# Performance work log

Measured on AMD Instinct MI355X. Metric: run time of the kernel, lower is better.

The kernel has to match this reference:

```python
import jax, jax.numpy as jnp
import numpy as np

BS = 16; N_PER = 1024; N = BS * N_PER; K = 9; E = N * K
H = 128; NODE_D = 64; EDGE_D = 16; RBF_DIM = 20; R_CUT = 1.0; L = 4; SF = 0.1


def setup_inputs():
    ks = jax.random.split(jax.random.key(0), 24)
    X = jax.random.normal(ks[0], (N, 3), dtype=jnp.float32) * 0.5
    node_attr = jax.random.normal(ks[1], (N, NODE_D), dtype=jnp.float32)
    edge_attr = jax.random.normal(ks[2], (E, EDGE_D), dtype=jnp.float32)
    idx = jnp.arange(N, dtype=jnp.int32)
    bid = idx // N_PER
    Seg = ((idx % N_PER) >= (N_PER // 2)).astype(jnp.int32)
    row = jnp.repeat(idx, K)
    col = (row // N_PER) * N_PER + jax.random.randint(ks[3], (E,), 0, N_PER, dtype=jnp.int32)
    edges = jnp.stack([row, col])

    def g(k, shape, fan):
        return jax.random.normal(k, shape, dtype=jnp.float32) * (1.0 / float(np.sqrt(fan)))

    MI = 2 * H + RBF_DIM + EDGE_D  # message MLP input dim
    return {
        'X': X, 'node_attr': node_attr, 'edge_attr': edge_attr,
        'W_in1': g(ks[4], (NODE_D, H), NODE_D), 'b_in1': jnp.zeros((H,), jnp.float32),
        'W_in2': g(ks[5], (H, H), H), 'b_in2': jnp.zeros((H,), jnp.float32),
        'We1': g(ks[6], (L, MI, H), MI), 'be1': jnp.zeros((L, H), jnp.float32),
        'We2': g(ks[7], (L, H, H), H), 'be2': jnp.zeros((L, H), jnp.float32),
        'Wv': g(ks[8], (L, H, H), H), 'Wvv': g(ks[9], (L, H, H), H),
        'Wh1': g(ks[10], (L, 2 * H, H), 2 * H), 'bh1': jnp.zeros((L, H), jnp.float32),
        'Wh2': g(ks[11], (L, H, H), H), 'bh2': jnp.zeros((L, H), jnp.float32),
        'Wi1': g(ks[12], (L, H, H), H), 'bi1': jnp.zeros((L, H), jnp.float32),
        'Wi2': g(ks[13], (L, H, H), H), 'bi2': jnp.zeros((L, H), jnp.float32),
        'Wgv1': g(ks[14], (H, H), H), 'Wgv2': g(ks[15], (H, H), H),
        'Wg1': g(ks[16], (2 * H, H), 2 * H), 'bg1': jnp.zeros((H,), jnp.float32),
        'Wg2': g(ks[17], (H, 2 * H), H), 'bg2': jnp.zeros((2 * H,), jnp.float32),
        'Wf': g(ks[18], (H, 9), H),
        'edges': edges, 'Seg': Seg, 'bid': bid,
    }


def _fwd(X, node_attr, edge_attr, W_in1, b_in1, W_in2, b_in2, We1, be1, We2, be2, Wv, Wvv, Wh1, bh1, Wh2, bh2, Wi1, bi1, Wi2, bi2, Wgv1, Wgv2, Wg1, bg1, Wg2, bg2, Wf, edges, Seg, bid):
    silu = jax.nn.silu
    row, col = edges[0], edges[1]
    nseg = 2 * BS
    seg_id = bid * 2 + Seg  # (complex, receptor/ligand) segment id
    # coord2radial + Bessel RBF with cosine cutoff
    diff = X[row] - X[col]
    norm = jnp.sqrt(jnp.sum(diff * diff, axis=-1)) + 1e-8
    unit = diff / norm[:, None]
    freqs = jnp.arange(1, RBF_DIM + 1, dtype=X.dtype) * (jnp.pi / R_CUT)
    rbf = jnp.sin(norm[:, None] * freqs[None, :]) / norm[:, None]
    cut = 0.5 * (jnp.cos(jnp.pi * jnp.clip(norm, 0.0, R_CUT) / R_CUT) + 1.0)
    rbf = rbf * cut[:, None]
    # in_conv
    h = silu(node_attr @ W_in1 + b_in1) @ W_in2 + b_in2
    v = jnp.zeros((N, H, 3), dtype=h.dtype)
    counts = jax.ops.segment_sum(jnp.ones((N,), dtype=h.dtype), seg_id, num_segments=nseg)
    opp = bid * 2 + (1 - Seg)  # opposite-molecule segment per node
    for i in range(L):
        # PINN message passing (PaiNN-style equivariant layer)
        m_in = jnp.concatenate([h[row], h[col], rbf, edge_attr], axis=-1)
        m = silu(m_in @ We1[i] + be1[i]) @ We2[i] + be2[i]  # [E, H]
        agg = jax.ops.segment_sum(m, row, num_segments=N)
        h_intra = h + silu(jnp.concatenate([h, agg], axis=-1) @ Wh1[i] + bh1[i]) @ Wh2[i] + bh2[i]
        v_msg = (m @ Wv[i])[:, :, None] * unit[:, None, :] + (m @ Wvv[i])[:, :, None] * v[col]
        v = v + jax.ops.segment_sum(v_msg, row, num_segments=N)
        # cross receptor<->ligand softmax attention: (H_a @ H_b.T).mean(1) == H_a @ mean(H_b)
        mean_h = jax.ops.segment_sum(h_intra, seg_id, num_segments=nseg) / counts[:, None]
        score = jnp.sum(h_intra * mean_h[opp], axis=-1)
        smax = jax.ops.segment_max(score, seg_id, num_segments=nseg)
        ex = jnp.exp(score - smax[seg_id])
        w = ex / jax.ops.segment_sum(ex, seg_id, num_segments=nseg)[seg_id]
        gated = h_intra * w[:, None]
        h = h_intra + silu(gated @ Wi1[i] + bi1[i]) @ Wi2[i] + bi2[i]
    # gated equivariant block
    v1 = jnp.einsum('nhc,hk->nkc', v, Wgv1)
    v2 = jnp.einsum('nhc,hk->nkc', v, Wgv2)
    v2n = jnp.sqrt(jnp.sum(v2 * v2, axis=-1) + 1e-8)
    mix = silu(jnp.concatenate([h, v2n], axis=-1) @ Wg1 + bg1) @ Wg2 + bg2
    h, bgate = mix[:, :H], mix[:, H:]
    v = v1 * bgate[:, :, None]
    # final_conv + per-(complex, molecule) pooled prediction vectors [2*BS, 9, 3]
    pv = jnp.einsum('nhc,ho->noc', v * h[:, :, None], Wf)
    pred = jax.ops.segment_sum(pv.reshape(N, 27), seg_id, num_segments=nseg).reshape(nseg, 9, 3)
    # kron/outer-product quadratic surface params: A [., 3, 3], b [., 3]
    A = (pred[:, 0, :, None] * pred[:, 1, None, :] + pred[:, 3, :, None] * pred[:, 2, None, :]
         + pred[:, 4, :, None] * pred[:, 5, None, :] + pred[:, 7, :, None] * pred[:, 6, None, :]) / (SF * SF)
    bvec = pred[:, 8] / SF
    return jnp.concatenate([A, bvec[:, :, None]], axis=2)  # [2*BS, 3, 4]


def reference(X, node_attr, edge_attr, W_in1, b_in1, W_in2, b_in2, We1, be1, We2, be2, Wv, Wvv, Wh1, bh1, Wh2, bh2, Wi1, bi1, Wi2, bi2, Wgv1, Wgv2, Wg1, bg1, Wg2, bg2, Wf, edges, Seg, bid):
    return _fwd(X, node_attr, edge_attr, W_in1, b_in1, W_in2, b_in2, We1, be1, We2, be2, Wv, Wvv, Wh1, bh1, Wh2, bh2, Wi1, bi1, Wi2, bi2, Wgv1, Wgv2, Wg1, bg1, Wg2, bg2, Wf, edges, Seg, bid)
```

## Files before the change

kernel.cpp:

```cpp
#include <hip/hip_runtime.h>
#include <math.h>

#define NN 16384
#define NE 147456
#define NSEGS 32
#define HD 128
#define RBF_D 20
#define EDGE_DD 16
#define NODE_DD 64
#define NLAYER 4
#define PI_F 3.14159265358979323846f


typedef __attribute__((ext_vector_type(8))) short v8s;
typedef __attribute__((ext_vector_type(4))) float v4f;
typedef __attribute__((ext_vector_type(8))) unsigned short v8u;

__device__ __forceinline__ unsigned short f2bf(float f) {
  union { float f; unsigned int u; } x; x.f = f;
  unsigned int u = x.u;
  return (unsigned short)((u + 0x7FFFu + ((u >> 16) & 1u)) >> 16);
}
__device__ __forceinline__ float bf2f(unsigned short b) {
  union { unsigned int u; float f; } x; x.u = ((unsigned int)b) << 16; return x.f;
}
__device__ __forceinline__ void split8(float4 a, float4 b, v8u& hi, v8u& lo) {
  float v[8] = {a.x, a.y, a.z, a.w, b.x, b.y, b.z, b.w};
#pragma unroll
  for (int i = 0; i < 8; i++) {
    unsigned short h = f2bf(v[i]);
    hi[i] = h;
    lo[i] = f2bf(v[i] - bf2f(h));
  }
}
__device__ __forceinline__ float silu_f(float v) { return v / (1.f + expf(-v)); }

struct WDesc { const float* src; const float* src2; unsigned short* hi; unsigned short* lo;
               int K; int N; int Kp; int ld; };
struct WDescs { WDesc d[48]; };
__global__ void wconv_k(WDescs ds) {
  WDesc d = ds.d[blockIdx.y];
  int idx = blockIdx.x * 256 + threadIdx.x;
  if (idx >= d.N * d.Kp) return;
  int n = idx / d.Kp, k = idx - n * d.Kp;
  const float* s = d.src; int nn = n;
  if (d.src2 && n >= 128) { s = d.src2; nn = n - 128; }
  float v = (k < d.K) ? s[(size_t)k * d.ld + nn] : 0.f;
  unsigned short h = f2bf(v);
  d.hi[idx] = h;
  d.lo[idx] = f2bf(v - bf2f(h));
}

__global__ void wcomb_k(const float* __restrict__ We2, const float* __restrict__ Wv,
                        const float* __restrict__ Wvv, float* __restrict__ Wc) {
  int l = blockIdx.z, which = blockIdx.y, xb = blockIdx.x;
  const float* A = We2 + (size_t)l * 128 * 128;
  const float* B = (which ? Wvv : Wv) + (size_t)l * 128 * 128;
  float* D = Wc + ((size_t)(which * NLAYER + l)) * 128 * 128;
  int n = threadIdx.x & 127, r2 = threadIdx.x >> 7;
#pragma unroll
  for (int i = 0; i < 8; i++) {
    int k1 = xb * 16 + r2 * 8 + i;
    float s = 0.f;
    for (int j = 0; j < 128; j++) s += A[k1 * 128 + j] * B[j * 128 + n];
    D[(size_t)k1 * 128 + n] = s;
  }
}
__global__ void bcomb_k(const float* __restrict__ be2, const float* __restrict__ Wv,
                        const float* __restrict__ Wvv, const float* __restrict__ be1,
                        float* __restrict__ bcv, float* __restrict__ bcvv,
                        float* __restrict__ b9, float* __restrict__ bx) {
  int l = blockIdx.x, n = threadIdx.x;
  const float* b = be2 + l * 128;
  float sv = 0.f, svv = 0.f;
  for (int j = 0; j < 128; j++) {
    sv  += b[j] * Wv[(size_t)l * 16384 + j * 128 + n];
    svv += b[j] * Wvv[(size_t)l * 16384 + j * 128 + n];
  }
  bcv[l * 128 + n] = sv; bcvv[l * 128 + n] = svv; b9[l * 128 + n] = 9.f * b[n];
  bx[l * 256 + n] = be1[l * 128 + n]; bx[l * 256 + 128 + n] = 0.f;
}

constexpr int LDS_S = 40;

template<int BM, int AMODE, int OUTM, int RESM>
__global__ __launch_bounds__(256, 2)
void mgemm_k(const float* A0f, const unsigned short* Ah0, const unsigned short* Al0,
             const unsigned short* __restrict__ Wth, const unsigned short* __restrict__ Wtl,
             int Kp, const float* __restrict__ bias, const float* __restrict__ resf,
             float* Cf, int ldc, unsigned short* Ch, unsigned short* Cl, int lda)
{
  constexpr int MT = BM / 32;
  __shared__ unsigned short Ah[BM * LDS_S], Al[BM * LDS_S];
  __shared__ unsigned short Bh[128 * LDS_S], Bl[128 * LDS_S];
  const int tid = threadIdx.x;
  const int m0 = blockIdx.x * BM;
  const int coff = blockIdx.y * 128;
  const int w = tid >> 6, lane = tid & 63;
  const int lm = lane & 15, kq = lane >> 4;
  const int wm = (w >> 1) * (BM / 2);
  const int wn = (w & 1) * 64;

  v4f acc[MT][4];
#pragma unroll
  for (int i = 0; i < MT; i++)
#pragma unroll
    for (int j = 0; j < 4; j++) acc[i][j] = (v4f){0.f, 0.f, 0.f, 0.f};

  const int KT = Kp >> 5;
  for (int kt = 0; kt < KT; kt++) {
#pragma unroll
    for (int i = 0; i < BM / 64; i++) {
      int m = i * 64 + (tid >> 2);
      int k8 = (tid & 3) * 8;
      int gk = kt * 32 + k8, gm = m0 + m;
      v8u hi, lo;
      if constexpr (AMODE == 1) {
        hi = *(const v8u*)&Ah0[(size_t)gm * 128 + gk];
        lo = *(const v8u*)&Al0[(size_t)gm * 128 + gk];
      } else {
        float4 a = *(const float4*)&A0f[(size_t)gm * lda + gk];
        float4 b = *(const float4*)&A0f[(size_t)gm * lda + gk + 4];
        split8(a, b, hi, lo);
      }
      *(v8u*)&Ah[m * LDS_S + k8] = hi;
      *(v8u*)&Al[m * LDS_S + k8] = lo;
    }
#pragma unroll
    for (int i = 0; i < 2; i++) {
      int f = i * 256 + tid;
      int n = f >> 2, k8 = (f & 3) * 8;
      size_t g = (size_t)(coff + n) * Kp + kt * 32 + k8;
      *(v8u*)&Bh[n * LDS_S + k8] = *(const v8u*)&Wth[g];
      *(v8u*)&Bl[n * LDS_S + k8] = *(const v8u*)&Wtl[g];
    }
    __syncthreads();
    v8s afh[MT], afl[MT];
#pragma unroll
    for (int mi = 0; mi < MT; mi++) {
      int r = wm + mi * 16 + lm;
      afh[mi] = *(v8s*)&Ah[r * LDS_S + kq * 8];
      afl[mi] = *(v8s*)&Al[r * LDS_S + kq * 8];
    }
#pragma unroll
    for (int ni = 0; ni < 4; ni++) {
      int r = wn + ni * 16 + lm;
      v8s bh = *(v8s*)&Bh[r * LDS_S + kq * 8];
      v8s bl = *(v8s*)&Bl[r * LDS_S + kq * 8];
#pragma unroll
      for (int mi = 0; mi < MT; mi++) {
        acc[mi][ni] = __builtin_amdgcn_mfma_f32_16x16x32_bf16(afh[mi], bh, acc[mi][ni], 0, 0, 0);
        acc[mi][ni] = __builtin_amdgcn_mfma_f32_16x16x32_bf16(afl[mi], bh, acc[mi][ni], 0, 0, 0);
        acc[mi][ni] = __builtin_amdgcn_mfma_f32_16x16x32_bf16(afh[mi], bl, acc[mi][ni], 0, 0, 0);
      }
    }
    __syncthreads();
  }
#pragma unroll
  for (int mi = 0; mi < MT; mi++) {
#pragma unroll
    for (int r = 0; r < 4; r++) {
      int mrow = m0 + wm + mi * 16 + kq * 4 + r;
#pragma unroll
      for (int ni = 0; ni < 4; ni++) {
        int ncol = coff + wn + ni * 16 + lm;
        float v = acc[mi][ni][r];
        if constexpr (RESM == 3) v += bias[ncol] * resf[mrow];
        else { if (bias) v += bias[ncol]; }
        if constexpr (OUTM == 0) Cf[(size_t)mrow * ldc + ncol] = v;
        else if constexpr (OUTM == 1) {
          unsigned short h = f2bf(v);
          Ch[(size_t)mrow * 128 + ncol] = h;
          Cl[(size_t)mrow * 128 + ncol] = f2bf(v - bf2f(h));
        } else {
          Ch[(size_t)mrow * 128 + ncol] = f2bf(v);
        }
      }
    }
  }
}

__device__ __forceinline__ float4 loadRE(const float* __restrict__ rbf,
                                         const float* __restrict__ ea, int m, int k4) {
  if (k4 < RBF_D) return *(const float4*)&rbf[(size_t)m * RBF_D + k4];
  if (k4 < RBF_D + EDGE_DD) return *(const float4*)&ea[(size_t)m * EDGE_DD + k4 - RBF_D];
  return make_float4(0.f, 0.f, 0.f, 0.f);
}

__global__ __launch_bounds__(256, 4)
void mrev_k(const float* __restrict__ rbf, const float* __restrict__ ea,
            const float* __restrict__ hrc, const float* __restrict__ unitv,
            const int* __restrict__ gcol,
            const unsigned short* __restrict__ W1h, const unsigned short* __restrict__ W1l,
            const unsigned short* __restrict__ W2h, const unsigned short* __restrict__ W2l,
            const float* __restrict__ bcvv,
            float* __restrict__ agg, float* __restrict__ U,
            unsigned short* __restrict__ mvvh)
{
  __shared__ unsigned short Th[64 * 136], Tl[64 * 136];
  __shared__ float su[192];
  unsigned short* Ah = Th;
  unsigned short* Al = Th + 64 * LDS_S;
  const int tid = threadIdx.x;
  const int m0 = blockIdx.x * 64;
  const int w = tid >> 6, lane = tid & 63;
  const int lm = lane & 15, kq = lane >> 4;
  const int wm = (w >> 1) * 32, wn = (w & 1) * 64;

  if (tid < 192) su[tid] = unitv[(size_t)m0 * 3 + tid];

  v4f acc[2][4];
#pragma unroll
  for (int i = 0; i < 2; i++)
#pragma unroll
    for (int j = 0; j < 4; j++) acc[i][j] = (v4f){0.f, 0.f, 0.f, 0.f};

  for (int kt = 0; kt < 2; kt++) {
    {
      int m = tid >> 2, k8 = (tid & 3) * 8;
      int gk = kt * 32 + k8, gm = m0 + m;
      v8u hi, lo;
      split8(loadRE(rbf, ea, gm, gk), loadRE(rbf, ea, gm, gk + 4), hi, lo);
      *(v8u*)&Ah[m * LDS_S + k8] = hi;
      *(v8u*)&Al[m * LDS_S + k8] = lo;
    }
    __syncthreads();
    v8s afh[2], afl[2];
#pragma unroll
    for (int mi = 0; mi < 2; mi++) {
      int r = wm + mi * 16 + lm;
      afh[mi] = *(v8s*)&Ah[r * LDS_S + kq * 8];
      afl[mi] = *(v8s*)&Al[r * LDS_S + kq * 8];
    }
#pragma unroll
    for (int ni = 0; ni < 4; ni++) {
      int n = wn + ni * 16 + lm;
      v8s bh = *(const v8s*)&W1h[(size_t)n * 64 + kt * 32 + kq * 8];
      v8s bl = *(const v8s*)&W1l[(size_t)n * 64 + kt * 32 + kq * 8];
#pragma unroll
      for (int mi = 0; mi < 2; mi++) {
        acc[mi][ni] = __builtin_amdgcn_mfma_f32_16x16x32_bf16(afh[mi], bh, acc[mi][ni], 0, 0, 0);
        acc[mi][ni] = __builtin_amdgcn_mfma_f32_16x16x32_bf16(afl[mi], bh, acc[mi][ni], 0, 0, 0);
        acc[mi][ni] = __builtin_amdgcn_mfma_f32_16x16x32_bf16(afh[mi], bl, acc[mi][ni], 0, 0, 0);
      }
    }
    __syncthreads();
  }
#pragma unroll
  for (int mi = 0; mi < 2; mi++) {
#pragma unroll
    for (int r = 0; r < 4; r++) {
      int row = wm + mi * 16 + kq * 4 + r;
      int e = m0 + row;
      const float* pr = hrc + (size_t)(e / 9) * 256;
      const float* pc = hrc + (size_t)gcol[e] * 256 + 128;
#pragma unroll
      for (int ni = 0; ni < 4; ni++) {
        int nc = wn + ni * 16 + lm;
        float v = silu_f(acc[mi][ni][r] + pr[nc] + pc[nc]);
        unsigned short h = f2bf(v);
        Th[row * 136 + nc] = h;
        Tl[row * 136 + nc] = f2bf(v - bf2f(h));
      }
    }
  }
  __syncthreads();
  {
    const size_t P = (size_t)NN * 128;
    int nfirst = m0 / 9;
#pragma unroll
    for (int it = 0; it < 4; it++) {
      int idx = it * 256 + tid;
      int ln = idx >> 7, c = idx & 127;
      int n = nfirst + ln;
      int r0 = n * 9 - m0, r1 = r0 + 9;
      if (r0 < 0) r0 = 0;
      if (r1 > 64) r1 = 64;
      float s = 0.f, u0 = 0.f, u1 = 0.f, u2 = 0.f;
      for (int r = r0; r < r1; r++) {
        float m = bf2f(Th[r * 136 + c]) + bf2f(Tl[r * 136 + c]);
        s += m;
        u0 += su[r * 3 + 0] * m;
        u1 += su[r * 3 + 1] * m;
        u2 += su[r * 3 + 2] * m;
      }
      if (r0 < r1) {
        size_t b = (size_t)n * 128 + c;
        atomicAdd(&agg[b], s);
        atomicAdd(&U[b], u0);
        atomicAdd(&U[P + b], u1);
        atomicAdd(&U[2 * P + b], u2);
      }
    }
  }
  v4f acc2[2][4];
#pragma unroll
  for (int i = 0; i < 2; i++)
#pragma unroll
    for (int j = 0; j < 4; j++) acc2[i][j] = (v4f){0.f, 0.f, 0.f, 0.f};
  for (int kt = 0; kt < 4; kt++) {
    v8s afh[2], afl[2];
#pragma unroll
    for (int mi = 0; mi < 2; mi++) {
      int r = wm + mi * 16 + lm;
      afh[mi] = *(v8s*)&Th[r * 136 + kt * 32 + kq * 8];
      afl[mi] = *(v8s*)&Tl[r * 136 + kt * 32 + kq * 8];
    }
#pragma unroll
    for (int ni = 0; ni < 4; ni++) {
      int n = wn + ni * 16 + lm;
      v8s bh = *(const v8s*)&W2h[(size_t)n * 128 + kt * 32 + kq * 8];
      v8s bl = *(const v8s*)&W2l[(size_t)n * 128 + kt * 32 + kq * 8];
#pragma unroll
      for (int mi = 0; mi < 2; mi++) {
        acc2[mi][ni] = __builtin_amdgcn_mfma_f32_16x16x32_bf16(afh[mi], bh, acc2[mi][ni], 0, 0, 0);
        acc2[mi][ni] = __builtin_amdgcn_mfma_f32_16x16x32_bf16(afl[mi], bh, acc2[mi][ni], 0, 0, 0);
        acc2[mi][ni] = __builtin_amdgcn_mfma_f32_16x16x32_bf16(afh[mi], bl, acc2[mi][ni], 0, 0, 0);
      }
    }
  }
#pragma unroll
  for (int mi = 0; mi < 2; mi++) {
#pragma unroll
    for (int r = 0; r < 4; r++) {
      int e = m0 + wm + mi * 16 + kq * 4 + r;
#pragma unroll
      for (int ni = 0; ni < 4; ni++) {
        int nc = wn + ni * 16 + lm;
        mvvh[(size_t)e * 128 + nc] = f2bf(acc2[mi][ni][r] + bcvv[nc]);
      }
    }
  }
}

template<int AMODE, int OUTM, int RESM>
__global__ __launch_bounds__(256, 2)
void mlp2_k(const float* A0f, const float* A1f,
            const unsigned short* Ah0, const unsigned short* Al0,
            const unsigned short* __restrict__ W1h, const unsigned short* __restrict__ W1l,
            int k1p, const float* __restrict__ b1,
            const unsigned short* __restrict__ W2h, const unsigned short* __restrict__ W2l,
            const float* __restrict__ b2,
            const float* resf, const unsigned short* resh, const unsigned short* resl,
            float* Cf, int ldc, unsigned short* Ch, unsigned short* Cl, int lda)
{
  __shared__ unsigned short Ah[64 * LDS_S], Al[64 * LDS_S];
  __shared__ unsigned short Bh[128 * LDS_S], Bl[128 * LDS_S];
  __shared__ unsigned short Th[64 * 136], Tl[64 * 136];
  const int tid = threadIdx.x;
  const int m0 = blockIdx.x * 64;
  const int w = tid >> 6, lane = tid & 63;
  const int lm = lane & 15, kq = lane >> 4;
  const int wm = (w >> 1) * 32, wn = (w & 1) * 64;

  v4f acc[2][4];
#pragma unroll
  for (int i = 0; i < 2; i++)
#pragma unroll
    for (int j = 0; j < 4; j++) acc[i][j] = (v4f){0.f, 0.f, 0.f, 0.f};

  for (int kt = 0; kt < (k1p >> 5); kt++) {
    {
      int m = tid >> 2, k8 = (tid & 3) * 8;
      int gk = kt * 32 + k8, gm = m0 + m;
      v8u hi, lo;
      if constexpr (AMODE == 3) {
        if (gk < 128) {
          hi = *(const v8u*)&Ah0[(size_t)gm * 128 + gk];
          lo = *(const v8u*)&Al0[(size_t)gm * 128 + gk];
        } else {
          float4 a = *(const float4*)&A1f[(size_t)gm * 128 + gk - 128];
          float4 b = *(const float4*)&A1f[(size_t)gm * 128 + gk - 124];
          split8(a, b, hi, lo);
        }
      } else {
        float4 a = *(const float4*)&A0f[(size_t)gm * lda + gk];
        float4 b = *(const float4*)&A0f[(size_t)gm * lda + gk + 4];
        if constexpr (AMODE == 4) {
          float s = A1f[gm];
          a.x *= s; a.y *= s; a.z *= s; a.w *= s;
          b.x *= s; b.y *= s; b.z *= s; b.w *= s;
        }
        split8(a, b, hi, lo);
      }
      *(v8u*)&Ah[m * LDS_S + k8] = hi;
      *(v8u*)&Al[m * LDS_S + k8] = lo;
    }
#pragma unroll
    for (int i = 0; i < 2; i++) {
      int f = i * 256 + tid;
      int n = f >> 2, k8 = (f & 3) * 8;
      size_t g = (size_t)n * k1p + kt * 32 + k8;
      *(v8u*)&Bh[n * LDS_S + k8] = *(const v8u*)&W1h[g];
      *(v8u*)&Bl[n * LDS_S + k8] = *(const v8u*)&W1l[g];
    }
    __syncthreads();
    v8s afh[2], afl[2];
#pragma unroll
    for (int mi = 0; mi < 2; mi++) {
      int r = wm + mi * 16 + lm;
      afh[mi] = *(v8s*)&Ah[r * LDS_S + kq * 8];
      afl[mi] = *(v8s*)&Al[r * LDS_S + kq * 8];
    }
#pragma unroll
    for (int ni = 0; ni < 4; ni++) {
      int r = wn + ni * 16 + lm;
      v8s bh = *(v8s*)&Bh[r * LDS_S + kq * 8];
      v8s bl = *(v8s*)&Bl[r * LDS_S + kq * 8];
#pragma unroll
      for (int mi = 0; mi < 2; mi++) {
        acc[mi][ni] = __builtin_amdgcn_mfma_f32_16x16x32_bf16(afh[mi], bh, acc[mi][ni], 0, 0, 0);
        acc[mi][ni] = __builtin_amdgcn_mfma_f32_16x16x32_bf16(afl[mi], bh, acc[mi][ni], 0, 0, 0);
        acc[mi][ni] = __builtin_amdgcn_mfma_f32_16x16x32_bf16(afh[mi], bl, acc[mi][ni], 0, 0, 0);
      }
    }
    __syncthreads();
  }
#pragma unroll
  for (int mi = 0; mi < 2; mi++) {
#pragma unroll
    for (int r = 0; r < 4; r++) {
      int row = wm + mi * 16 + kq * 4 + r;
#pragma unroll
      for (int ni = 0; ni < 4; ni++) {
        int col = wn + ni * 16 + lm;
        float v = silu_f(acc[mi][ni][r] + b1[col]);
        unsigned short h = f2bf(v);
        Th[row * 136 + col] = h;
        Tl[row * 136 + col] = f2bf(v - bf2f(h));
      }
    }
  }
  __syncthreads();
  const int coff2 = blockIdx.y * 128;
  v4f acc2[2][4];
#pragma unroll
  for (int i = 0; i < 2; i++)
#pragma unroll
    for (int j = 0; j < 4; j++) acc2[i][j] = (v4f){0.f, 0.f, 0.f, 0.f};
  for (int kt = 0; kt < 4; kt++) {
#pragma unroll
    for (int i = 0; i < 2; i++) {
      int f = i * 256 + tid;
      int n = f >> 2, k8 = (f & 3) * 8;
      size_t g = (size_t)(coff2 + n) * 128 + kt * 32 + k8;
      *(v8u*)&Bh[n * LDS_S + k8] = *(const v8u*)&W2h[g];
      *(v8u*)&Bl[n * LDS_S + k8] = *(const v8u*)&W2l[g];
    }
    __syncthreads();
    v8s afh[2], afl[2];
#pragma unroll
    for (int mi = 0; mi < 2; mi++) {
      int r = wm + mi * 16 + lm;
      afh[mi] = *(v8s*)&Th[r * 136 + kt * 32 + kq * 8];
      afl[mi] = *(v8s*)&Tl[r * 136 + kt * 32 + kq * 8];
    }
#pragma unroll
    for (int ni = 0; ni < 4; ni++) {
      int r = wn + ni * 16 + lm;
      v8s bh = *(v8s*)&Bh[r * LDS_S + kq * 8];
      v8s bl = *(v8s*)&Bl[r * LDS_S + kq * 8];
#pragma unroll
      for (int mi = 0; mi < 2; mi++) {
        acc2[mi][ni] = __builtin_amdgcn_mfma_f32_16x16x32_bf16(afh[mi], bh, acc2[mi][ni], 0, 0, 0);
        acc2[mi][ni] = __builtin_amdgcn_mfma_f32_16x16x32_bf16(afl[mi], bh, acc2[mi][ni], 0, 0, 0);
        acc2[mi][ni] = __builtin_amdgcn_mfma_f32_16x16x32_bf16(afh[mi], bl, acc2[mi][ni], 0, 0, 0);
      }
    }
    __syncthreads();
  }
#pragma unroll
  for (int mi = 0; mi < 2; mi++) {
#pragma unroll
    for (int r = 0; r < 4; r++) {
      int mrow = m0 + wm + mi * 16 + kq * 4 + r;
#pragma unroll
      for (int ni = 0; ni < 4; ni++) {
        int ncol = coff2 + wn + ni * 16 + lm;
        float v = acc2[mi][ni][r];
        if (b2) v += b2[ncol];
        if constexpr (RESM == 1) v += resf[(size_t)mrow * 128 + ncol];
        if constexpr (RESM == 2) v += bf2f(resh[(size_t)mrow * 128 + ncol]) + bf2f(resl[(size_t)mrow * 128 + ncol]);
        if constexpr (OUTM == 0) Cf[(size_t)mrow * ldc + ncol] = v;
        else {
          unsigned short h = f2bf(v);
          Ch[(size_t)mrow * 128 + ncol] = h;
          Cl[(size_t)mrow * 128 + ncol] = f2bf(v - bf2f(h));
        }
      }
    }
  }
}

__global__ void edge_geom_k(const float* __restrict__ X, const int* __restrict__ row,
                            const int* __restrict__ col,
                            float* __restrict__ unitv, float* __restrict__ rbf) {
  int e = blockIdx.x * 256 + threadIdx.x;
  if (e >= NE) return;
  int r = row[e], c = col[e];
  float dx = X[r * 3 + 0] - X[c * 3 + 0];
  float dy = X[r * 3 + 1] - X[c * 3 + 1];
  float dz = X[r * 3 + 2] - X[c * 3 + 2];
  float norm = sqrtf(dx * dx + dy * dy + dz * dz) + 1e-8f;
  float inv = 1.f / norm;
  unitv[e * 3 + 0] = dx * inv;
  unitv[e * 3 + 1] = dy * inv;
  unitv[e * 3 + 2] = dz * inv;
  float cl = fminf(norm, 1.0f);
  float cut = 0.5f * (cosf(PI_F * cl) + 1.0f);
  float s = cut * inv;
#pragma unroll
  for (int j = 0; j < RBF_D; j++) rbf[(size_t)e * RBF_D + j] = sinf(norm * (float)(j + 1) * PI_F) * s;
}

__global__ void sup_k(const float* __restrict__ unitv, float* __restrict__ sup) {
  int n = blockIdx.x * 256 + threadIdx.x;
  if (n >= NN) return;
  float q0 = 0.f, q1 = 0.f, q2 = 0.f;
#pragma unroll
  for (int k = 0; k < 9; k++) {
    const float* u = &unitv[(size_t)(n * 9 + k) * 3];
    q0 += u[0]; q1 += u[1]; q2 += u[2];
  }
  sup[n] = q0; sup[NN + n] = q1; sup[2 * NN + n] = q2;
}

__global__ void vupd_k(const float* __restrict__ vold, const float* __restrict__ t1,
                       const unsigned short* __restrict__ mvvh,
                       const int* __restrict__ col, float* __restrict__ vnew) {
  const size_t P = (size_t)NN * 128;
  int t = blockIdx.x * 256 + threadIdx.x;
  int n = t >> 7, hh = t & 127;
  size_t b = (size_t)n * 128 + hh;
  float a0 = vold[b] + t1[b];
  float a1 = vold[P + b] + t1[P + b];
  float a2 = vold[2 * P + b] + t1[2 * P + b];
#pragma unroll
  for (int k = 0; k < 9; k++) {
    int e = n * 9 + k;
    int ce = col[e];
    float mvv = bf2f(mvvh[(size_t)e * 128 + hh]);
    size_t cb = (size_t)ce * 128 + hh;
    a0 += mvv * vold[cb];
    a1 += mvv * vold[P + cb];
    a2 += mvv * vold[2 * P + cb];
  }
  vnew[b] = a0; vnew[P + b] = a1; vnew[2 * P + b] = a2;
}

__global__ void meanp_k(const float* __restrict__ hintra, float* __restrict__ meanp) {
  int q = blockIdx.x, s = blockIdx.y, c = threadIdx.x;
  const float* p = hintra + ((size_t)s * 512 + q * 64) * 128 + c;
// ... 132 lines not shown
  const int* rowp = edges;
  const int* colp = edges + NE;
  float* out = (float*)d_out;

  char* ws = (char*)d_ws;
  size_t o = 0;
  auto ab = [&](size_t bytes) { char* p = ws + o; o += (bytes + 255) & ~(size_t)255; return p; };
  float* unitv  = (float*)ab((size_t)NE * 3 * 4);
  float* rbf    = (float*)ab((size_t)NE * RBF_D * 4);
  float* va     = (float*)ab((size_t)NN * 384 * 4);
  float* vb     = (float*)ab((size_t)NN * 384 * 4);
  unsigned short* mvvh = (unsigned short*)ab((size_t)NE * 128 * 2);
  float* hrc    = (float*)ab((size_t)NN * 256 * 4);
  float* U      = (float*)ab((size_t)3 * NN * 128 * 4);
  float* agg    = (float*)ab((size_t)NN * 128 * 4);
  float* sup    = (float*)ab((size_t)3 * NN * 4);
  float* hintra = (float*)ab((size_t)NN * 128 * 4);
  unsigned short* hbh = (unsigned short*)ab((size_t)NN * 128 * 2);
  unsigned short* hbl = (unsigned short*)ab((size_t)NN * 128 * 2);
  float* meanp  = (float*)ab(NSEGS * 8 * 128 * 4);
  float* scoreb = (float*)ab(NN * 4);
  float* wgt    = (float*)ab(NN * 4);
  float* pred   = (float*)ab(NSEGS * 27 * 4);
  float* Wc     = (float*)ab((size_t)2 * NLAYER * 128 * 128 * 4);
  float* bcv    = (float*)ab(NLAYER * 128 * 4);
  float* bcvv   = (float*)ab(NLAYER * 128 * 4);
  float* b9     = (float*)ab(NLAYER * 128 * 4);
  float* bx     = (float*)ab(NLAYER * 256 * 4);
  unsigned short* wt = (unsigned short*)ab(4 * 1024 * 1024);
  float* v12  = (float*)mvvh;
  float* mixb = (float*)U;

  size_t wo = 0;
  auto walloc = [&](size_t n) { unsigned short* p = wt + wo; wo += n; return p; };
  WDescs wd{};
  int wcnt = 0;
  auto addw = [&](const float* src, const float* src2, int K, int N, int Kp, int ld) {
    size_t sz = (size_t)N * Kp;
    unsigned short* hi = walloc(sz);
    unsigned short* lo = walloc(sz);
    wd.d[wcnt] = WDesc{src, src2, hi, lo, K, N, Kp, ld};
    return wcnt++;
  };
  int iWin1 = addw(W_in1, nullptr, 64, 128, 64, 128);
  int iWin2 = addw(W_in2, nullptr, 128, 128, 128, 128);
  int iWe1rc[NLAYER], iWe1re[NLAYER], iWe2[NLAYER], iWcv[NLAYER], iWcvv[NLAYER],
      iWh1[NLAYER], iWh2[NLAYER], iWi1[NLAYER], iWi2[NLAYER];
  for (int i = 0; i < NLAYER; i++) {
    const float* Wl = We1 + (size_t)i * 292 * 128;
    iWe1rc[i] = addw(Wl, Wl + 128 * 128, 128, 256, 128, 128);
    iWe1re[i] = addw(Wl + 256 * 128, nullptr, 36, 128, 64, 128);
    iWe2[i]   = addw(We2 + (size_t)i * 16384, nullptr, 128, 128, 128, 128);
    iWcv[i]   = addw(Wc + (size_t)i * 16384, nullptr, 128, 128, 128, 128);
    iWcvv[i]  = addw(Wc + (size_t)(NLAYER + i) * 16384, nullptr, 128, 128, 128, 128);
    iWh1[i]   = addw(Wh1 + (size_t)i * 256 * 128, nullptr, 256, 128, 256, 128);
    iWh2[i]   = addw(Wh2 + (size_t)i * 16384, nullptr, 128, 128, 128, 128);
    iWi1[i]   = addw(Wi1 + (size_t)i * 16384, nullptr, 128, 128, 128, 128);
    iWi2[i]   = addw(Wi2 + (size_t)i * 16384, nullptr, 128, 128, 128, 128);
  }
  int iWg1   = addw(Wg1, nullptr, 256, 128, 256, 128);
  int iWg2   = addw(Wg2, nullptr, 128, 256, 128, 256);
  int iWgv12 = addw(Wgv1, Wgv2, 128, 256, 128, 128);

  hipMemsetAsync(va, 0, (size_t)NN * 384 * sizeof(float), stream);
  hipMemsetAsync(pred, 0, NSEGS * 27 * sizeof(float), stream);

  wcomb_k<<<dim3(8, 2, NLAYER), 256, 0, stream>>>(We2, Wv, Wvv, Wc);
  bcomb_k<<<NLAYER, 128, 0, stream>>>(be2, Wv, Wvv, be1, bcv, bcvv, b9, bx);
  wconv_k<<<dim3(128, wcnt), 256, 0, stream>>>(wd);
  edge_geom_k<<<NE / 256, 256, 0, stream>>>(X, rowp, colp, unitv, rbf);
  sup_k<<<NN / 256, 256, 0, stream>>>(unitv, sup);

  auto WH = [&](int idx) { return wd.d[idx].hi; };
  auto WL = [&](int idx) { return wd.d[idx].lo; };

  mlp2_k<0, 1, 0><<<dim3(NN / 64, 1), 256, 0, stream>>>(
      node_attr, nullptr, nullptr, nullptr,
      WH(iWin1), WL(iWin1), 64, b_in1, WH(iWin2), WL(iWin2), b_in2,
      nullptr, nullptr, nullptr, nullptr, 128, hbh, hbl, NODE_DD);

  float* vcur = va;
  float* vnxt = vb;
  for (int i = 0; i < NLAYER; i++) {
    hipMemsetAsync(U, 0, (size_t)4 * NN * 128 * sizeof(float), stream);
    mgemm_k<64, 1, 0, 0><<<dim3(NN / 64, 2), 256, 0, stream>>>(
        nullptr, hbh, hbl, WH(iWe1rc[i]), WL(iWe1rc[i]), 128,
        bx + i * 256, nullptr, hrc, 256, nullptr, nullptr, 0);
    mrev_k<<<NE / 64, 256, 0, stream>>>(rbf, edge_attr, hrc, unitv, colp,
        WH(iWe1re[i]), WL(iWe1re[i]), WH(iWcvv[i]), WL(iWcvv[i]),
        bcvv + i * 128, agg, U, mvvh);
    mgemm_k<64, 0, 0, 0><<<dim3(NN / 64, 1), 256, 0, stream>>>(
        agg, nullptr, nullptr, WH(iWe2[i]), WL(iWe2[i]), 128,
        b9 + i * 128, nullptr, agg, 128, nullptr, nullptr, 128);
    mlp2_k<3, 0, 2><<<dim3(NN / 64, 1), 256, 0, stream>>>(
        nullptr, agg, hbh, hbl,
        WH(iWh1[i]), WL(iWh1[i]), 256, bh1 + i * 128, WH(iWh2[i]), WL(iWh2[i]), bh2 + i * 128,
        nullptr, hbh, hbl, hintra, 128, nullptr, nullptr, 0);
    meanp_k<<<dim3(8, NSEGS), 128, 0, stream>>>(hintra, meanp);
    score2_k<<<NN / 4, 256, 0, stream>>>(hintra, meanp, scoreb);
    softmax_k<<<NSEGS, 512, 0, stream>>>(scoreb, wgt);
    mgemm_k<64, 0, 0, 3><<<dim3(3 * NN / 64, 1), 256, 0, stream>>>(
        U, nullptr, nullptr, WH(iWcv[i]), WL(iWcv[i]), 128,
        bcv + i * 128, sup, U, 128, nullptr, nullptr, 128);
    vupd_k<<<NN * 128 / 256, 256, 0, stream>>>(vcur, U, mvvh, colp, vnxt);
    { float* t = vcur; vcur = vnxt; vnxt = t; }
    mlp2_k<4, 1, 1><<<dim3(NN / 64, 1), 256, 0, stream>>>(
        hintra, wgt, nullptr, nullptr,
        WH(iWi1[i]), WL(iWi1[i]), 128, bi1 + i * 128, WH(iWi2[i]), WL(iWi2[i]), bi2 + i * 128,
        hintra, nullptr, nullptr, nullptr, 128, hbh, hbl, 128);
  }

  mgemm_k<64, 0, 0, 0><<<dim3(3 * NN / 64, 2), 256, 0, stream>>>(
      vcur, nullptr, nullptr, WH(iWgv12), WL(iWgv12), 128,
      nullptr, nullptr, v12, 256, nullptr, nullptr, 128);
  v2n_k<<<NN * 128 / 256, 256, 0, stream>>>(v12, agg);
  mlp2_k<3, 0, 0><<<dim3(NN / 64, 2), 256, 0, stream>>>(
      nullptr, agg, hbh, hbl,
      WH(iWg1), WL(iWg1), 256, bg1, WH(iWg2), WL(iWg2), bg2,
      nullptr, nullptr, nullptr, mixb, 256, nullptr, nullptr, 0);
  pv_k<<<NN / 8, 256, 0, stream>>>(v12, mixb, Wf, pred);
  out_k<<<1, 64, 0, stream>>>(pred, out);
}
```

Before: 1.142 ms.

## Load GEMM fragments directly from global memory, dropping LDS staging and barriers

```diff
diff --git a/kernel.cpp b/kernel.cpp
--- a/kernel.cpp
+++ b/kernel.cpp
@@ -81,83 +81,57 @@
   bx[l * 256 + n] = be1[l * 128 + n]; bx[l * 256 + 128 + n] = 0.f;
 }
 
-constexpr int LDS_S = 40;
-
-template<int BM, int AMODE, int OUTM, int RESM>
-__global__ __launch_bounds__(256, 2)
+template<int AMODE, int OUTM, int RESM>
+__global__ __launch_bounds__(256, 4)
 void mgemm_k(const float* A0f, const unsigned short* Ah0, const unsigned short* Al0,
              const unsigned short* __restrict__ Wth, const unsigned short* __restrict__ Wtl,
              int Kp, const float* __restrict__ bias, const float* __restrict__ resf,
              float* Cf, int ldc, unsigned short* Ch, unsigned short* Cl, int lda)
 {
-  constexpr int MT = BM / 32;
-  __shared__ unsigned short Ah[BM * LDS_S], Al[BM * LDS_S];
-  __shared__ unsigned short Bh[128 * LDS_S], Bl[128 * LDS_S];
-  const int tid = threadIdx.x;
-  const int m0 = blockIdx.x * BM;
+  const int m0 = blockIdx.x * 64;
   const int coff = blockIdx.y * 128;
-  const int w = tid >> 6, lane = tid & 63;
+  const int w = threadIdx.x >> 6, lane = threadIdx.x & 63;
   const int lm = lane & 15, kq = lane >> 4;
-  const int wm = (w >> 1) * (BM / 2);
-  const int wn = (w & 1) * 64;
-
-  v4f acc[MT][4];
-#pragma unroll
-  for (int i = 0; i < MT; i++)
+  const int wm = (w >> 1) * 32, wn = (w & 1) * 64;
+
+  v4f acc[2][4];
+#pragma unroll
+  for (int i = 0; i < 2; i++)
 #pragma unroll
     for (int j = 0; j < 4; j++) acc[i][j] = (v4f){0.f, 0.f, 0.f, 0.f};
 
-  const int KT = Kp >> 5;
-  for (int kt = 0; kt < KT; kt++) {
-#pragma unroll
-    for (int i = 0; i < BM / 64; i++) {
-      int m = i * 64 + (tid >> 2);
-      int k8 = (tid & 3) * 8;
-      int gk = kt * 32 + k8, gm = m0 + m;
-      v8u hi, lo;
+  for (int kt = 0; kt < (Kp >> 5); kt++) {
+    v8s afh[2], afl[2];
+#pragma unroll
+    for (int mi = 0; mi < 2; mi++) {
+      int row = m0 + wm + mi * 16 + lm;
+      int gk = kt * 32 + kq * 8;
       if constexpr (AMODE == 1) {
-        hi = *(const v8u*)&Ah0[(size_t)gm * 128 + gk];
-        lo = *(const v8u*)&Al0[(size_t)gm * 128 + gk];
+        afh[mi] = *(const v8s*)&Ah0[(size_t)row * 128 + gk];
+        afl[mi] = *(const v8s*)&Al0[(size_t)row * 128 + gk];
       } else {
-        float4 a = *(const float4*)&A0f[(size_t)gm * lda + gk];
-        float4 b = *(const float4*)&A0f[(size_t)gm * lda + gk + 4];
+        float4 a = *(const float4*)&A0f[(size_t)row * lda + gk];
+        float4 b = *(const float4*)&A0f[(size_t)row * lda + gk + 4];
+        v8u hi, lo;
         split8(a, b, hi, lo);
-      }
-      *(v8u*)&Ah[m * LDS_S + k8] = hi;
-      *(v8u*)&Al[m * LDS_S + k8] = lo;
-    }
-#pragma unroll
-    for (int i = 0; i < 2; i++) {
-      int f = i * 256 + tid;
-      int n = f >> 2, k8 = (f & 3) * 8;
-      size_t g = (size_t)(coff + n) * Kp + kt * 32 + k8;
-      *(v8u*)&Bh[n * LDS_S + k8] = *(const v8u*)&Wth[g];
-      *(v8u*)&Bl[n * LDS_S + k8] = *(const v8u*)&Wtl[g];
-    }
-    __syncthreads();
-    v8s afh[MT], afl[MT];
-#pragma unroll
-    for (int mi = 0; mi < MT; mi++) {
-      int r = wm + mi * 16 + lm;
-      afh[mi] = *(v8s*)&Ah[r * LDS_S + kq * 8];
-      afl[mi] = *(v8s*)&Al[r * LDS_S + kq * 8];
+        afh[mi] = (v8s)hi; afl[mi] = (v8s)lo;
+      }
     }
 #pragma unroll
     for (int ni = 0; ni < 4; ni++) {
-      int r = wn + ni * 16 + lm;
-      v8s bh = *(v8s*)&Bh[r * LDS_S + kq * 8];
-      v8s bl = *(v8s*)&Bl[r * LDS_S + kq * 8];
-#pragma unroll
-      for (int mi = 0; mi < MT; mi++) {
+      int n = coff + wn + ni * 16 + lm;
+      v8s bh = *(const v8s*)&Wth[(size_t)n * Kp + kt * 32 + kq * 8];
+      v8s bl = *(const v8s*)&Wtl[(size_t)n * Kp + kt * 32 + kq * 8];
+#pragma unroll
+      for (int mi = 0; mi < 2; mi++) {
         acc[mi][ni] = __builtin_amdgcn_mfma_f32_16x16x32_bf16(afh[mi], bh, acc[mi][ni], 0, 0, 0);
         acc[mi][ni] = __builtin_amdgcn_mfma_f32_16x16x32_bf16(afl[mi], bh, acc[mi][ni], 0, 0, 0);
         acc[mi][ni] = __builtin_amdgcn_mfma_f32_16x16x32_bf16(afh[mi], bl, acc[mi][ni], 0, 0, 0);
       }
     }
-    __syncthreads();
-  }
-#pragma unroll
-  for (int mi = 0; mi < MT; mi++) {
+  }
+#pragma unroll
+  for (int mi = 0; mi < 2; mi++) {
 #pragma unroll
     for (int r = 0; r < 4; r++) {
       int mrow = m0 + wm + mi * 16 + kq * 4 + r;
@@ -168,12 +142,10 @@
         if constexpr (RESM == 3) v += bias[ncol] * resf[mrow];
         else { if (bias) v += bias[ncol]; }
         if constexpr (OUTM == 0) Cf[(size_t)mrow * ldc + ncol] = v;
-        else if constexpr (OUTM == 1) {
+        else {
           unsigned short h = f2bf(v);
           Ch[(size_t)mrow * 128 + ncol] = h;
           Cl[(size_t)mrow * 128 + ncol] = f2bf(v - bf2f(h));
-        } else {
-          Ch[(size_t)mrow * 128 + ncol] = f2bf(v);
         }
       }
     }
@@ -199,8 +171,6 @@
 {
   __shared__ unsigned short Th[64 * 136], Tl[64 * 136];
   __shared__ float su[192];
-  unsigned short* Ah = Th;
-  unsigned short* Al = Th + 64 * LDS_S;
   const int tid = threadIdx.x;
   const int m0 = blockIdx.x * 64;
   const int w = tid >> 6, lane = tid & 63;
@@ -215,22 +185,16 @@
 #pragma unroll
     for (int j = 0; j < 4; j++) acc[i][j] = (v4f){0.f, 0.f, 0.f, 0.f};
 
+#pragma unroll
   for (int kt = 0; kt < 2; kt++) {
-    {
-      int m = tid >> 2, k8 = (tid & 3) * 8;
-      int gk = kt * 32 + k8, gm = m0 + m;
+    v8s afh[2], afl[2];
+#pragma unroll
+    for (int mi = 0; mi < 2; mi++) {
+      int row = m0 + wm + mi * 16 + lm;
+      int gk = kt * 32 + kq * 8;
       v8u hi, lo;
-      split8(loadRE(rbf, ea, gm, gk), loadRE(rbf, ea, gm, gk + 4), hi, lo);
-      *(v8u*)&Ah[m * LDS_S + k8] = hi;
-      *(v8u*)&Al[m * LDS_S + k8] = lo;
-    }
-    __syncthreads();
-    v8s afh[2], afl[2];
-#pragma unroll
-    for (int mi = 0; mi < 2; mi++) {
-      int r = wm + mi * 16 + lm;
-      afh[mi] = *(v8s*)&Ah[r * LDS_S + kq * 8];
-      afl[mi] = *(v8s*)&Al[r * LDS_S + kq * 8];
+      split8(loadRE(rbf, ea, row, gk), loadRE(rbf, ea, row, gk + 4), hi, lo);
+      afh[mi] = (v8s)hi; afl[mi] = (v8s)lo;
     }
 #pragma unroll
     for (int ni = 0; ni < 4; ni++) {
@@ -244,7 +208,6 @@
         acc[mi][ni] = __builtin_amdgcn_mfma_f32_16x16x32_bf16(afh[mi], bl, acc[mi][ni], 0, 0, 0);
       }
     }
-    __syncthreads();
   }
 #pragma unroll
   for (int mi = 0; mi < 2; mi++) {
@@ -274,6 +237,7 @@
       int ln = idx >> 7, c = idx & 127;
       int n = nfirst + ln;
       int r0 = n * 9 - m0, r1 = r0 + 9;
+      bool interior = (r0 >= 0) && (r1 <= 64);
       if (r0 < 0) r0 = 0;
       if (r1 > 64) r1 = 64;
       float s = 0.f, u0 = 0.f, u1 = 0.f, u2 = 0.f;
@@ -286,10 +250,14 @@
       }
       if (r0 < r1) {
         size_t b = (size_t)n * 128 + c;
-        atomicAdd(&agg[b], s);
-        atomicAdd(&U[b], u0);
-        atomicAdd(&U[P + b], u1);
-        atomicAdd(&U[2 * P + b], u2);
+        if (interior) {
+          agg[b] = s; U[b] = u0; U[P + b] = u1; U[2 * P + b] = u2;
+        } else {
+          atomicAdd(&agg[b], s);
+          atomicAdd(&U[b], u0);
+          atomicAdd(&U[P + b], u1);
+          atomicAdd(&U[2 * P + b], u2);
+        }
       }
     }
   }
@@ -334,7 +302,7 @@
 }
 
 template<int AMODE, int OUTM, int RESM>
-__global__ __launch_bounds__(256, 2)
+__global__ __launch_bounds__(256, 4)
 void mlp2_k(const float* A0f, const float* A1f,
             const unsigned short* Ah0, const unsigned short* Al0,
             const unsigned short* __restrict__ W1h, const unsigned short* __restrict__ W1l,
@@ -344,8 +312,6 @@
             const float* resf, const unsigned short* resh, const unsigned short* resl,
             float* Cf, int ldc, unsigned short* Ch, unsigned short* Cl, int lda)
 {
-  __shared__ unsigned short Ah[64 * LDS_S], Al[64 * LDS_S];
-  __shared__ unsigned short Bh[128 * LDS_S], Bl[128 * LDS_S];
   __shared__ unsigned short Th[64 * 136], Tl[64 * 136];
   const int tid = threadIdx.x;
   const int m0 = blockIdx.x * 64;
@@ -360,53 +326,38 @@
     for (int j = 0; j < 4; j++) acc[i][j] = (v4f){0.f, 0.f, 0.f, 0.f};
 
   for (int kt = 0; kt < (k1p >> 5); kt++) {
-    {
-      int m = tid >> 2, k8 = (tid & 3) * 8;
-      int gk = kt * 32 + k8, gm = m0 + m;
-      v8u hi, lo;
+    v8s afh[2], afl[2];
+#pragma unroll
+    for (int mi = 0; mi < 2; mi++) {
+      int row = m0 + wm + mi * 16 + lm;
+      int gk = kt * 32 + kq * 8;
       if constexpr (AMODE == 3) {
         if (gk < 128) {
-          hi = *(const v8u*)&Ah0[(size_t)gm * 128 + gk];
-          lo = *(const v8u*)&Al0[(size_t)gm * 128 + gk];
+          afh[mi] = *(const v8s*)&Ah0[(size_t)row * 128 + gk];
+          afl[mi] = *(const v8s*)&Al0[(size_t)row * 128 + gk];
         } else {
-          float4 a = *(const float4*)&A1f[(size_t)gm * 128 + gk - 128];
-          float4 b = *(const float4*)&A1f[(size_t)gm * 128 + gk - 124];
-          split8(a, b, hi, lo);
+          float4 a = *(const float4*)&A1f[(size_t)row * 128 + gk - 128];
+          float4 b = *(const float4*)&A1f[(size_t)row * 128 + gk - 124];
+          v8u hi, lo; split8(a, b, hi, lo);
+          afh[mi] = (v8s)hi; afl[mi] = (v8s)lo;
         }
       } else {
-        float4 a = *(const float4*)&A0f[(size_t)gm * lda + gk];
-        float4 b = *(const float4*)&A0f[(size_t)gm * lda + gk + 4];
+        float4 a = *(const float4*)&A0f[(size_t)row * lda + gk];
+        float4 b = *(const float4*)&A0f[(size_t)row * lda + gk + 4];
         if constexpr (AMODE == 4) {
-          float s = A1f[gm];
+          float s = A1f[row];
           a.x *= s; a.y *= s; a.z *= s; a.w *= s;
           b.x *= s; b.y *= s; b.z *= s; b.w *= s;
         }
-        split8(a, b, hi, lo);
-      }
-      *(v8u*)&Ah[m * LDS_S + k8] = hi;
-      *(v8u*)&Al[m * LDS_S + k8] = lo;
-    }
-#pragma unroll
-    for (int i = 0; i < 2; i++) {
-      int f = i * 256 + tid;
-      int n = f >> 2, k8 = (f & 3) * 8;
-      size_t g = (size_t)n * k1p + kt * 32 + k8;
-      *(v8u*)&Bh[n * LDS_S + k8] = *(const v8u*)&W1h[g];
-      *(v8u*)&Bl[n * LDS_S + k8] = *(const v8u*)&W1l[g];
-    }
-    __syncthreads();
-    v8s afh[2], afl[2];
-#pragma unroll
-    for (int mi = 0; mi < 2; mi++) {
-      int r = wm + mi * 16 + lm;
-      afh[mi] = *(v8s*)&Ah[r * LDS_S + kq * 8];
-      afl[mi] = *(v8s*)&Al[r * LDS_S + kq * 8];
+        v8u hi, lo; split8(a, b, hi, lo);
+        afh[mi] = (v8s)hi; afl[mi] = (v8s)lo;
+      }
     }
 #pragma unroll
     for (int ni = 0; ni < 4; ni++) {
-      int r = wn + ni * 16 + lm;
-      v8s bh = *(v8s*)&Bh[r * LDS_S + kq * 8];
-      v8s bl = *(v8s*)&Bl[r * LDS_S + kq * 8];
+      int n = wn + ni * 16 + lm;
+      v8s bh = *(const v8s*)&W1h[(size_t)n * k1p + kt * 32 + kq * 8];
+      v8s bl = *(const v8s*)&W1l[(size_t)n * k1p + kt * 32 + kq * 8];
 #pragma unroll
       for (int mi = 0; mi < 2; mi++) {
         acc[mi][ni] = __builtin_amdgcn_mfma_f32_16x16x32_bf16(afh[mi], bh, acc[mi][ni], 0, 0, 0);
@@ -414,7 +365,6 @@
         acc[mi][ni] = __builtin_amdgcn_mfma_f32_16x16x32_bf16(afh[mi], bl, acc[mi][ni], 0, 0, 0);
       }
     }
-    __syncthreads();
   }
 #pragma unroll
   for (int mi = 0; mi < 2; mi++) {
@@ -439,15 +389,6 @@
 #pragma unroll
     for (int j = 0; j < 4; j++) acc2[i][j] = (v4f){0.f, 0.f, 0.f, 0.f};
   for (int kt = 0; kt < 4; kt++) {
-#pragma unroll
-    for (int i = 0; i < 2; i++) {
-      int f = i * 256 + tid;
-      int n = f >> 2, k8 = (f & 3) * 8;
-      size_t g = (size_t)(coff2 + n) * 128 + kt * 32 + k8;
-      *(v8u*)&Bh[n * LDS_S + k8] = *(const v8u*)&W2h[g];
-      *(v8u*)&Bl[n * LDS_S + k8] = *(const v8u*)&W2l[g];
-    }
-    __syncthreads();
     v8s afh[2], afl[2];
 #pragma unroll
     for (int mi = 0; mi < 2; mi++) {
@@ -457,9 +398,9 @@
     }
 #pragma unroll
     for (int ni = 0; ni < 4; ni++) {
-      int r = wn + ni * 16 + lm;
-      v8s bh = *(v8s*)&Bh[r * LDS_S + kq * 8];
-      v8s bl = *(v8s*)&Bl[r * LDS_S + kq * 8];
+      int n = coff2 + wn + ni * 16 + lm;
+      v8s bh = *(const v8s*)&W2h[(size_t)n * 128 + kt * 32 + kq * 8];
+      v8s bl = *(const v8s*)&W2l[(size_t)n * 128 + kt * 32 + kq * 8];
 #pragma unroll
       for (int mi = 0; mi < 2; mi++) {
         acc2[mi][ni] = __builtin_amdgcn_mfma_f32_16x16x32_bf16(afh[mi], bh, acc2[mi][ni], 0, 0, 0);
@@ -467,7 +408,6 @@
         acc2[mi][ni] = __builtin_amdgcn_mfma_f32_16x16x32_bf16(afh[mi], bl, acc2[mi][ni], 0, 0, 0);
       }
     }
-    __syncthreads();
   }
 #pragma unroll
   for (int mi = 0; mi < 2; mi++) {
@@ -767,13 +707,13 @@
   float* vnxt = vb;
   for (int i = 0; i < NLAYER; i++) {
     hipMemsetAsync(U, 0, (size_t)4 * NN * 128 * sizeof(float), stream);
-    mgemm_k<64, 1, 0, 0><<<dim3(NN / 64, 2), 256, 0, stream>>>(
+    mgemm_k<1, 0, 0><<<dim3(NN / 64, 2), 256, 0, stream>>>(
         nullptr, hbh, hbl, WH(iWe1rc[i]), WL(iWe1rc[i]), 128,
         bx + i * 256, nullptr, hrc, 256, nullptr, nullptr, 0);
     mrev_k<<<NE / 64, 256, 0, stream>>>(rbf, edge_attr, hrc, unitv, colp,
         WH(iWe1re[i]), WL(iWe1re[i]), WH(iWcvv[i]), WL(iWcvv[i]),
         bcvv + i * 128, agg, U, mvvh);
-    mgemm_k<64, 0, 0, 0><<<dim3(NN / 64, 1), 256, 0, stream>>>(
+    mgemm_k<0, 0, 0><<<dim3(NN / 64, 1), 256, 0, stream>>>(
         agg, nullptr, nullptr, WH(iWe2[i]), WL(iWe2[i]), 128,
         b9 + i * 128, nullptr, agg, 128, nullptr, nullptr, 128);
     mlp2_k<3, 0, 2><<<dim3(NN / 64, 1), 256, 0, stream>>>(
@@ -783,7 +723,7 @@
     meanp_k<<<dim3(8, NSEGS), 128, 0, stream>>>(hintra, meanp);
     score2_k<<<NN / 4, 256, 0, stream>>>(hintra, meanp, scoreb);
     softmax_k<<<NSEGS, 512, 0, stream>>>(scoreb, wgt);
-    mgemm_k<64, 0, 0, 3><<<dim3(3 * NN / 64, 1), 256, 0, stream>>>(
+    mgemm_k<0, 0, 3><<<dim3(3 * NN / 64, 1), 256, 0, stream>>>(
         U, nullptr, nullptr, WH(iWcv[i]), WL(iWcv[i]), 128,
         bcv + i * 128, sup, U, 128, nullptr, nullptr, 128);
     vupd_k<<<NN * 128 / 256, 256, 0, stream>>>(vcur, U, mvvh, colp, vnxt);
@@ -794,7 +734,7 @@
         hintra, nullptr, nullptr, nullptr, 128, hbh, hbl, 128);
   }
 
-  mgemm_k<64, 0, 0, 0><<<dim3(3 * NN / 64, 2), 256, 0, stream>>>(
+  mgemm_k<0, 0, 0><<<dim3(3 * NN / 64, 2), 256, 0, stream>>>(
       vcur, nullptr, nullptr, WH(iWgv12), WL(iWgv12), 128,
       nullptr, nullptr, v12, 256, nullptr, nullptr, 128);
   v2n_k<<<NN * 128 / 256, 256, 0, stream>>>(v12, agg);
```

Result: slower. 1.290 ms (+12.9%).

## Replace full memset with boundary-only zeroing and plain stores for interior node sums

Applied to the files above, without the earlier changes.

```diff
diff --git a/kernel.cpp b/kernel.cpp
--- a/kernel.cpp
+++ b/kernel.cpp
@@ -81,38 +81,47 @@
   bx[l * 256 + n] = be1[l * 128 + n]; bx[l * 256 + 128 + n] = 0.f;
 }
 
+__global__ void zerob_k(float* __restrict__ agg, float* __restrict__ U) {
+  int t = blockIdx.x * 256 + threadIdx.x;
+  int k = (t >> 7) + 1;
+  int c = t & 127;
+  if (k >= NE / 64) return;
+  int nk = 64 * k;
+  if (nk % 9 == 0) return;
+  int n = nk / 9;
+  const size_t P = (size_t)NN * 128;
+  size_t b = (size_t)n * 128 + c;
+  agg[b] = 0.f; U[b] = 0.f; U[P + b] = 0.f; U[2 * P + b] = 0.f;
+}
+
 constexpr int LDS_S = 40;
 
-template<int BM, int AMODE, int OUTM, int RESM>
-__global__ __launch_bounds__(256, 2)
+template<int AMODE, int OUTM, int RESM>
+__global__ __launch_bounds__(256, 4)
 void mgemm_k(const float* A0f, const unsigned short* Ah0, const unsigned short* Al0,
              const unsigned short* __restrict__ Wth, const unsigned short* __restrict__ Wtl,
              int Kp, const float* __restrict__ bias, const float* __restrict__ resf,
              float* Cf, int ldc, unsigned short* Ch, unsigned short* Cl, int lda)
 {
-  constexpr int MT = BM / 32;
-  __shared__ unsigned short Ah[BM * LDS_S], Al[BM * LDS_S];
+  __shared__ unsigned short Ah[64 * LDS_S], Al[64 * LDS_S];
   __shared__ unsigned short Bh[128 * LDS_S], Bl[128 * LDS_S];
   const int tid = threadIdx.x;
-  const int m0 = blockIdx.x * BM;
+  const int m0 = blockIdx.x * 64;
   const int coff = blockIdx.y * 128;
   const int w = tid >> 6, lane = tid & 63;
   const int lm = lane & 15, kq = lane >> 4;
-  const int wm = (w >> 1) * (BM / 2);
-  const int wn = (w & 1) * 64;
-
-  v4f acc[MT][4];
-#pragma unroll
-  for (int i = 0; i < MT; i++)
+  const int wm = (w >> 1) * 32, wn = (w & 1) * 64;
+
+  v4f acc[2][4];
+#pragma unroll
+  for (int i = 0; i < 2; i++)
 #pragma unroll
     for (int j = 0; j < 4; j++) acc[i][j] = (v4f){0.f, 0.f, 0.f, 0.f};
 
   const int KT = Kp >> 5;
   for (int kt = 0; kt < KT; kt++) {
-#pragma unroll
-    for (int i = 0; i < BM / 64; i++) {
-      int m = i * 64 + (tid >> 2);
-      int k8 = (tid & 3) * 8;
+    {
+      int m = tid >> 2, k8 = (tid & 3) * 8;
       int gk = kt * 32 + k8, gm = m0 + m;
       v8u hi, lo;
       if constexpr (AMODE == 1) {
@@ -135,9 +144,9 @@
       *(v8u*)&Bl[n * LDS_S + k8] = *(const v8u*)&Wtl[g];
     }
     __syncthreads();
-    v8s afh[MT], afl[MT];
-#pragma unroll
-    for (int mi = 0; mi < MT; mi++) {
+    v8s afh[2], afl[2];
+#pragma unroll
+    for (int mi = 0; mi < 2; mi++) {
       int r = wm + mi * 16 + lm;
       afh[mi] = *(v8s*)&Ah[r * LDS_S + kq * 8];
       afl[mi] = *(v8s*)&Al[r * LDS_S + kq * 8];
@@ -148,7 +157,7 @@
       v8s bh = *(v8s*)&Bh[r * LDS_S + kq * 8];
       v8s bl = *(v8s*)&Bl[r * LDS_S + kq * 8];
 #pragma unroll
-      for (int mi = 0; mi < MT; mi++) {
+      for (int mi = 0; mi < 2; mi++) {
         acc[mi][ni] = __builtin_amdgcn_mfma_f32_16x16x32_bf16(afh[mi], bh, acc[mi][ni], 0, 0, 0);
         acc[mi][ni] = __builtin_amdgcn_mfma_f32_16x16x32_bf16(afl[mi], bh, acc[mi][ni], 0, 0, 0);
         acc[mi][ni] = __builtin_amdgcn_mfma_f32_16x16x32_bf16(afh[mi], bl, acc[mi][ni], 0, 0, 0);
@@ -157,7 +166,7 @@
     __syncthreads();
   }
 #pragma unroll
-  for (int mi = 0; mi < MT; mi++) {
+  for (int mi = 0; mi < 2; mi++) {
 #pragma unroll
     for (int r = 0; r < 4; r++) {
       int mrow = m0 + wm + mi * 16 + kq * 4 + r;
@@ -168,12 +177,10 @@
         if constexpr (RESM == 3) v += bias[ncol] * resf[mrow];
         else { if (bias) v += bias[ncol]; }
         if constexpr (OUTM == 0) Cf[(size_t)mrow * ldc + ncol] = v;
-        else if constexpr (OUTM == 1) {
+        else {
           unsigned short h = f2bf(v);
           Ch[(size_t)mrow * 128 + ncol] = h;
           Cl[(size_t)mrow * 128 + ncol] = f2bf(v - bf2f(h));
-        } else {
-          Ch[(size_t)mrow * 128 + ncol] = f2bf(v);
         }
       }
     }
@@ -269,27 +276,40 @@
     const size_t P = (size_t)NN * 128;
     int nfirst = m0 / 9;
 #pragma unroll
-    for (int it = 0; it < 4; it++) {
+    for (int it = 0; it < 2; it++) {
       int idx = it * 256 + tid;
-      int ln = idx >> 7, c = idx & 127;
+      int ln = idx >> 6, cp = idx & 63;
+      int c = cp * 2;
       int n = nfirst + ln;
       int r0 = n * 9 - m0, r1 = r0 + 9;
+      bool interior = (r0 >= 0) && (r1 <= 64);
       if (r0 < 0) r0 = 0;
       if (r1 > 64) r1 = 64;
-      float s = 0.f, u0 = 0.f, u1 = 0.f, u2 = 0.f;
+      float s0 = 0, s1 = 0, u00 = 0, u01 = 0, u10 = 0, u11 = 0, u20 = 0, u21 = 0;
       for (int r = r0; r < r1; r++) {
-        float m = bf2f(Th[r * 136 + c]) + bf2f(Tl[r * 136 + c]);
-        s += m;
-        u0 += su[r * 3 + 0] * m;
-        u1 += su[r * 3 + 1] * m;
-        u2 += su[r * 3 + 2] * m;
+        ushort2 mh = *(const ushort2*)&Th[r * 136 + c];
+        ushort2 ml = *(const ushort2*)&Tl[r * 136 + c];
+        float mv0 = bf2f(mh.x) + bf2f(ml.x);
+        float mv1 = bf2f(mh.y) + bf2f(ml.y);
+        float su0 = su[r * 3 + 0], su1 = su[r * 3 + 1], su2 = su[r * 3 + 2];
+        s0 += mv0; s1 += mv1;
+        u00 += su0 * mv0; u01 += su0 * mv1;
+        u10 += su1 * mv0; u11 += su1 * mv1;
+        u20 += su2 * mv0; u21 += su2 * mv1;
       }
       if (r0 < r1) {
         size_t b = (size_t)n * 128 + c;
-        atomicAdd(&agg[b], s);
-        atomicAdd(&U[b], u0);
-        atomicAdd(&U[P + b], u1);
-        atomicAdd(&U[2 * P + b], u2);
+        if (interior) {
+          *(float2*)&agg[b]         = make_float2(s0, s1);
+          *(float2*)&U[b]           = make_float2(u00, u01);
+          *(float2*)&U[P + b]       = make_float2(u10, u11);
+          *(float2*)&U[2 * P + b]   = make_float2(u20, u21);
+        } else {
+          atomicAdd(&agg[b], s0);        atomicAdd(&agg[b + 1], s1);
+          atomicAdd(&U[b], u00);         atomicAdd(&U[b + 1], u01);
+          atomicAdd(&U[P + b], u10);     atomicAdd(&U[P + b + 1], u11);
+          atomicAdd(&U[2 * P + b], u20); atomicAdd(&U[2 * P + b + 1], u21);
+        }
       }
     }
   }
@@ -766,14 +786,14 @@
   float* vcur = va;
   float* vnxt = vb;
   for (int i = 0; i < NLAYER; i++) {
-    hipMemsetAsync(U, 0, (size_t)4 * NN * 128 * sizeof(float), stream);
-    mgemm_k<64, 1, 0, 0><<<dim3(NN / 64, 2), 256, 0, stream>>>(
+    zerob_k<<<1152, 256, 0, stream>>>(agg, U);
+    mgemm_k<1, 0, 0><<<dim3(NN / 64, 2), 256, 0, stream>>>(
         nullptr, hbh, hbl, WH(iWe1rc[i]), WL(iWe1rc[i]), 128,
         bx + i * 256, nullptr, hrc, 256, nullptr, nullptr, 0);
     mrev_k<<<NE / 64, 256, 0, stream>>>(rbf, edge_attr, hrc, unitv, colp,
         WH(iWe1re[i]), WL(iWe1re[i]), WH(iWcvv[i]), WL(iWcvv[i]),
         bcvv + i * 128, agg, U, mvvh);
-    mgemm_k<64, 0, 0, 0><<<dim3(NN / 64, 1), 256, 0, stream>>>(
+    mgemm_k<0, 0, 0><<<dim3(NN / 64, 1), 256, 0, stream>>>(
         agg, nullptr, nullptr, WH(iWe2[i]), WL(iWe2[i]), 128,
         b9 + i * 128, nullptr, agg, 128, nullptr, nullptr, 128);
     mlp2_k<3, 0, 2><<<dim3(NN / 64, 1), 256, 0, stream>>>(
@@ -783,7 +803,7 @@
     meanp_k<<<dim3(8, NSEGS), 128, 0, stream>>>(hintra, meanp);
     score2_k<<<NN / 4, 256, 0, stream>>>(hintra, meanp, scoreb);
     softmax_k<<<NSEGS, 512, 0, stream>>>(scoreb, wgt);
-    mgemm_k<64, 0, 0, 3><<<dim3(3 * NN / 64, 1), 256, 0, stream>>>(
+    mgemm_k<0, 0, 3><<<dim3(3 * NN / 64, 1), 256, 0, stream>>>(
         U, nullptr, nullptr, WH(iWcv[i]), WL(iWcv[i]), 128,
         bcv + i * 128, sup, U, 128, nullptr, nullptr, 128);
     vupd_k<<<NN * 128 / 256, 256, 0, stream>>>(vcur, U, mvvh, colp, vnxt);
@@ -794,7 +814,7 @@
         hintra, nullptr, nullptr, nullptr, 128, hbh, hbl, 128);
   }
 
-  mgemm_k<64, 0, 0, 0><<<dim3(3 * NN / 64, 2), 256, 0, stream>>>(
+  mgemm_k<0, 0, 0><<<dim3(3 * NN / 64, 2), 256, 0, stream>>>(
       vcur, nullptr, nullptr, WH(iWgv12), WL(iWgv12), 128,
       nullptr, nullptr, v12, 256, nullptr, nullptr, 128);
   v2n_k<<<NN * 128 / 256, 256, 0, stream>>>(v12, agg);
```

Measured after the change: 1.108 ms. 3.0% less time.
